# Kernel optimization log

Measured on AMD Instinct MI355X. Metric: run time of the kernel, lower is better.

## Reference

```python
import jax, jax.numpy as jnp
import numpy as np

N_PTS = 50000
EMBED = 192
HEADS = 12
HEAD_DIM = EMBED // HEADS          # 16
HPP = HEADS // 3                   # heads per strip plane = 4
QUANT = 0.25
QGL = 8                            # quant_grid_length = window/quant
TBL = 2 * QGL - 1                  # 15
BOX = 16.0
WS_XY = np.array([2.0, 2.0, 1.0], np.float32)
WS_XZ = np.array([2.0, 1.0, 2.0], np.float32)
WS_YZ = np.array([1.0, 2.0, 2.0], np.float32)


def _build_idx(xyz, ws):
    # padded per-window gather indices: equivalent of get_indices_params
    n = xyz.shape[0]
    sh = xyz - xyz.min(0)
    w = np.floor(sh / ws).astype(np.int64)
    key = (w[:, 0] * 100000 + w[:, 1]) * 100000 + w[:, 2]
    uniq, inv, counts = np.unique(key, return_inverse=True, return_counts=True)
    order = np.argsort(inv, kind='stable')
    starts = np.cumsum(counts) - counts
    pos = np.arange(n) - starts[inv[order]]
    idx = np.full((len(uniq), int(counts.max())), n, dtype=np.int32)  # pad = n
    idx[inv[order], pos] = order.astype(np.int32)
    return idx


def setup_inputs() -> dict:
    rng = np.random.default_rng(0)
    xyz = rng.uniform(0.0, BOX, (N_PTS, 3)).astype(np.float32)
    feats = rng.standard_normal((N_PTS, EMBED)).astype(np.float32)
    tbl = lambda: jnp.asarray((rng.standard_normal((TBL, 3, HPP, HEAD_DIM)) * 0.02).astype(np.float32))
    return {
        'feats': jnp.asarray(feats),
        'xyz': jnp.asarray(xyz),
        'idx_xy': jnp.asarray(_build_idx(xyz, WS_XY)),
        'idx_xz': jnp.asarray(_build_idx(xyz, WS_XZ)),
        'idx_yz': jnp.asarray(_build_idx(xyz, WS_YZ)),
        'W_qkv': jnp.asarray((rng.standard_normal((EMBED, 3 * EMBED)) * 0.02).astype(np.float32)),
        'b_qkv': jnp.zeros((3 * EMBED,), jnp.float32),
        'q_table': tbl(),
        'k_table': tbl(),
        'v_table': tbl(),
        'W_proj': jnp.asarray((rng.standard_normal((EMBED, EMBED)) * 0.02).astype(np.float32)),
        'b_proj': jnp.zeros((EMBED,), jnp.float32),
    }


def _plane_attention(q, k, v, xyz, idx, ws, qt, kt, vt):
    # q,k,v: [N,h,hd]; idx: [W,M] padded window membership (pad index == N)
    n, h, hd = q.shape
    Wn, M = idx.shape
    # quantized in-window coordinates (get_relative_position_index)
    qc = jnp.floor(((xyz - xyz.min(0)) % ws) / QUANT).astype(jnp.int32)
    pad = lambda a: jnp.concatenate([a, jnp.zeros((1,) + a.shape[1:], a.dtype)], axis=0)
    Q, K, V, QC = pad(q)[idx], pad(k)[idx], pad(v)[idx], pad(qc)[idx]
    mask = idx < n                                  # [W,M] valid slots
    rel = QC[:, :, None, :] - QC[:, None, :, :] + (QGL - 1)   # [W,M,M,3]
    logits = jnp.einsum('wmhd,wnhd->wmnh', Q, K)
    # per-slot dot products with every table row, gathered per pair
    qb = jnp.einsum('wmhd,lthd->wmtlh', Q, qt)      # [W,M,3,TBL,h]
    kb = jnp.einsum('wnhd,lthd->wntlh', K, kt)
    for t in range(3):
        r = rel[..., t]                             # [W,M,M]
        logits = logits + jnp.take_along_axis(qb[:, :, t], r[..., None], axis=2)
        rk = jnp.swapaxes(r, 1, 2)[..., None]       # index by key slot
        logits = logits + jnp.swapaxes(jnp.take_along_axis(kb[:, :, t], rk, axis=2), 1, 2)
    logits = jnp.where(mask[:, None, :, None], logits, -1e9)
    attn = jax.nn.softmax(logits, axis=2)           # [W,M,M,h]
    out = jnp.einsum('wmnh,wnhd->wmhd', attn, V)
    # relative-position value table: out_i += sum_n attn_in * v_table[rel_in]
    row = jnp.arange(Wn * M, dtype=jnp.int32).reshape(Wn, M)
    for t in range(3):
        ids = row[:, :, None] * TBL + rel[..., t]
        cb = jax.ops.segment_sum(attn.reshape(-1, h), ids.reshape(-1),
                                 num_segments=Wn * M * TBL)
        out = out + jnp.einsum('wmlh,lhd->wmhd', cb.reshape(Wn, M, TBL, h), vt[:, t])
    out = out * mask[..., None, None]
    acc = jnp.zeros((n + 1, h, hd), out.dtype).at[idx.reshape(-1)].add(out.reshape(-1, h, hd))
    return acc[:n]


def reference(feats, xyz, idx_xy, idx_xz, idx_yz, W_qkv, b_qkv,
              q_table, k_table, v_table, W_proj, b_proj):
    n = feats.shape[0]
    scale = HEAD_DIM ** -0.5
    qkv = (feats @ W_qkv + b_qkv).reshape(n, 3, HEADS, HEAD_DIM)
    q, k, v = qkv[:, 0] * scale, qkv[:, 1], qkv[:, 2]
    planes = [(idx_xy, jnp.asarray(WS_XY)), (idx_xz, jnp.asarray(WS_XZ)), (idx_yz, jnp.asarray(WS_YZ))]
    outs = []
    for p, (idx, ws) in enumerate(planes):
        sl = slice(p * HPP, (p + 1) * HPP)
        outs.append(_plane_attention(q[:, sl], k[:, sl], v[:, sl], xyz, idx, ws,
                                     q_table, k_table, v_table))
    x = jnp.concatenate(outs, axis=1).reshape(n, EMBED)
    return x @ W_proj + b_proj
```

## Files before the change

### kernel.cpp

```cpp
#include <hip/hip_runtime.h>
#include <math.h>

typedef __attribute__((ext_vector_type(8))) short bf16x8;
typedef __attribute__((ext_vector_type(4))) float f32x4;

union U16 { uint4 u; bf16x8 b; ushort s[8]; };

__device__ __forceinline__ ushort f2bf_rne(float f) {
  unsigned u = __float_as_uint(f);
  unsigned r = u + 0x7fffu + ((u >> 16) & 1u);
  return (ushort)(r >> 16);
}
__device__ __forceinline__ float bf2f(ushort h) {
  return __uint_as_float((unsigned)h << 16);
}

__global__ void min_init_kernel(unsigned* minb) {
  if (threadIdx.x < 3) minb[threadIdx.x] = 0x7f800000u;
}

__global__ void min_reduce_kernel(const float* __restrict__ xyz, unsigned* minb, int n) {
  float m0 = 1e30f, m1 = 1e30f, m2 = 1e30f;
  for (int i = blockIdx.x * blockDim.x + threadIdx.x; i < n; i += gridDim.x * blockDim.x) {
    m0 = fminf(m0, xyz[3 * i + 0]);
    m1 = fminf(m1, xyz[3 * i + 1]);
    m2 = fminf(m2, xyz[3 * i + 2]);
  }
#pragma unroll
  for (int off = 32; off > 0; off >>= 1) {
    m0 = fminf(m0, __shfl_down(m0, off, 64));
    m1 = fminf(m1, __shfl_down(m1, off, 64));
    m2 = fminf(m2, __shfl_down(m2, off, 64));
  }
  if ((threadIdx.x & 63) == 0) {
    atomicMin(&minb[0], __float_as_uint(m0));
    atomicMin(&minb[1], __float_as_uint(m1));
    atomicMin(&minb[2], __float_as_uint(m2));
  }
}

__global__ void prep_w_kernel(const float* __restrict__ W, short* __restrict__ Wh,
                              short* __restrict__ Wl, int K, int Ncols) {
  int idx = blockIdx.x * 256 + threadIdx.x;
  if (idx >= K * Ncols) return;
  int n = idx / K, k = idx - n * K;
  float v = W[(size_t)k * Ncols + n];
  ushort h = f2bf_rne(v);
  Wh[idx] = (short)h;
  Wl[idx] = (short)f2bf_rne(v - bf2f(h));
}

__global__ __launch_bounds__(256, 2) void mfma_gemm_kernel(
    const float* __restrict__ A, const short* __restrict__ Bh_g, const short* __restrict__ Bl_g,
    const float* __restrict__ bias, float* __restrict__ C, ushort* __restrict__ Cb,
    int Mrows, int Ncols, int K, int mode)
{
  __shared__ short Ah[128][40];
  __shared__ short Al[128][40];
  __shared__ short Bsh[128][40];
  __shared__ short Bsl[128][40];
  const int tid = threadIdx.x;
  const int lane = tid & 63;
  const int w = tid >> 6;
  const int wm = w >> 1, wn = w & 1;
  const int rowBase = blockIdx.y * 128;
  const int colBase = blockIdx.x * 128;

  f32x4 acc[4][4];
#pragma unroll
  for (int i = 0; i < 4; ++i)
#pragma unroll
    for (int j = 0; j < 4; ++j)
      acc[i][j] = (f32x4){0.f, 0.f, 0.f, 0.f};

  const int ma = tid >> 3;
  const int ka = (tid & 7) * 4;
  const int fr = lane & 15;
  const int kq = (lane >> 4) * 8;

  for (int k0 = 0; k0 < K; k0 += 32) {
    __syncthreads();
#pragma unroll
    for (int i = 0; i < 4; ++i) {
      int m = ma + 32 * i;
      int gr = rowBase + m;
      float4 v = make_float4(0.f, 0.f, 0.f, 0.f);
      if (gr < Mrows) v = *(const float4*)&A[(size_t)gr * K + k0 + ka];
      ushort h0 = f2bf_rne(v.x), h1 = f2bf_rne(v.y), h2 = f2bf_rne(v.z), h3 = f2bf_rne(v.w);
      ushort l0 = f2bf_rne(v.x - bf2f(h0));
      ushort l1 = f2bf_rne(v.y - bf2f(h1));
      ushort l2 = f2bf_rne(v.z - bf2f(h2));
      ushort l3 = f2bf_rne(v.w - bf2f(h3));
      uint2 hw, lw;
      hw.x = (unsigned)h0 | ((unsigned)h1 << 16);
      hw.y = (unsigned)h2 | ((unsigned)h3 << 16);
      lw.x = (unsigned)l0 | ((unsigned)l1 << 16);
      lw.y = (unsigned)l2 | ((unsigned)l3 << 16);
      *(uint2*)&Ah[m][ka] = hw;
      *(uint2*)&Al[m][ka] = lw;
    }
#pragma unroll
    for (int i = 0; i < 2; ++i) {
      int s = tid + 256 * i;
      int n = s >> 2;
      int k8 = (s & 3) * 8;
      int gn = colBase + n;
      if (gn >= Ncols) gn = Ncols - 1;
      *(uint4*)&Bsh[n][k8] = *(const uint4*)&Bh_g[(size_t)gn * K + k0 + k8];
      *(uint4*)&Bsl[n][k8] = *(const uint4*)&Bl_g[(size_t)gn * K + k0 + k8];
    }
    __syncthreads();
    bf16x8 afh[4], afl[4], bfh[4], bfl[4];
#pragma unroll
    for (int t = 0; t < 4; ++t) {
      int r = wm * 64 + t * 16 + fr;
      afh[t] = *(const bf16x8*)&Ah[r][kq];
      afl[t] = *(const bf16x8*)&Al[r][kq];
      int c = wn * 64 + t * 16 + fr;
      bfh[t] = *(const bf16x8*)&Bsh[c][kq];
      bfl[t] = *(const bf16x8*)&Bsl[c][kq];
    }
#pragma unroll
    for (int mt = 0; mt < 4; ++mt)
#pragma unroll
      for (int nt = 0; nt < 4; ++nt) {
        acc[mt][nt] = __builtin_amdgcn_mfma_f32_16x16x32_bf16(afh[mt], bfh[nt], acc[mt][nt], 0, 0, 0);
        acc[mt][nt] = __builtin_amdgcn_mfma_f32_16x16x32_bf16(afh[mt], bfl[nt], acc[mt][nt], 0, 0, 0);
        acc[mt][nt] = __builtin_amdgcn_mfma_f32_16x16x32_bf16(afl[mt], bfh[nt], acc[mt][nt], 0, 0, 0);
      }
  }
  const int cr = (lane >> 4) * 4;
  const int ccol = lane & 15;
#pragma unroll
  for (int mt = 0; mt < 4; ++mt) {
#pragma unroll
    for (int nt = 0; nt < 4; ++nt) {
      int col = colBase + wn * 64 + nt * 16 + ccol;
      if (col >= Ncols) continue;
      float bv = bias[col];
      float sc = (mode == 1 && col < 192) ? 0.25f : 1.0f;
#pragma unroll
      for (int r = 0; r < 4; ++r) {
        int row = rowBase + wm * 64 + mt * 16 + cr + r;
        if (row >= Mrows) continue;
        float val = (acc[mt][nt][r] + bv) * sc;
        if (mode == 1) Cb[(size_t)row * Ncols + col] = f2bf_rne(val);
        else C[(size_t)row * Ncols + col] = val;
      }
    }
  }
}

__global__ __launch_bounds__(256) void augment_mfma_kernel(
    const ushort* __restrict__ qkv_bf, const float* __restrict__ xyz,
    const unsigned* __restrict__ minb,
    const float* __restrict__ qt, const float* __restrict__ kt,
    ushort* __restrict__ QBg, ushort* __restrict__ KBg, ushort* __restrict__ qcg, int N)
{
  __shared__ ushort sQ[4][64 * 48 + 16];
  __shared__ ushort sKb[4][64 * 48 + 16];
  const int tid = threadIdx.x;
  const int lane = tid & 63;
  const int h = tid >> 6;
  const int p = blockIdx.y;
  const int n0 = blockIdx.x * 64;
  const int fc = lane & 15;
  const int qd = lane >> 4;

  bf16x8 tqh[3], tql[3], tkh[3], tkl[3];
#pragma unroll
  for (int ct = 0; ct < 3; ++ct) {
    U16 qh_, ql_, kh_, kl_;
    qh_.u = make_uint4(0u, 0u, 0u, 0u); ql_.u = qh_.u; kh_.u = qh_.u; kl_.u = qh_.u;
    int col = ct * 16 + fc;
    if (col < 45 && qd < 2) {
      int l = col / 3, t3 = col - l * 3;
      const float* qp = qt + (((l * 3 + t3) * 4 + h) * 16) + qd * 8;
      const float* kp = kt + (((l * 3 + t3) * 4 + h) * 16) + qd * 8;
#pragma unroll
      for (int j = 0; j < 8; ++j) {
        float qv = qp[j], kv = kp[j];
        ushort qhh = f2bf_rne(qv);
        qh_.s[j] = qhh; ql_.s[j] = f2bf_rne(qv - bf2f(qhh));
        ushort khh = f2bf_rne(kv);
        kh_.s[j] = khh; kl_.s[j] = f2bf_rne(kv - bf2f(khh));
      }
    }
    tqh[ct] = qh_.b; tql[ct] = ql_.b; tkh[ct] = kh_.b; tkl[ct] = kl_.b;
  }

#pragma unroll
  for (int mt = 0; mt < 4; ++mt) {
    int n = n0 + mt * 16 + fc;
    if (n >= N) n = N - 1;
    U16 qa, ka;
    qa.u = make_uint4(0u, 0u, 0u, 0u); ka.u = qa.u;
    if (qd < 2) {
      const ushort* base = qkv_bf + (size_t)n * 576 + p * 64 + h * 16 + qd * 8;
      qa.u = *(const uint4*)base;
      ka.u = *(const uint4*)(base + 192);
    }
#pragma unroll
    for (int ct = 0; ct < 3; ++ct) {
      f32x4 aq = (f32x4){0.f, 0.f, 0.f, 0.f}, ak = aq;
      aq = __builtin_amdgcn_mfma_f32_16x16x32_bf16(qa.b, tqh[ct], aq, 0, 0, 0);
      aq = __builtin_amdgcn_mfma_f32_16x16x32_bf16(qa.b, tql[ct], aq, 0, 0, 0);
      ak = __builtin_amdgcn_mfma_f32_16x16x32_bf16(ka.b, tkh[ct], ak, 0, 0, 0);
      ak = __builtin_amdgcn_mfma_f32_16x16x32_bf16(ka.b, tkl[ct], ak, 0, 0, 0);
#pragma unroll
      for (int i = 0; i < 4; ++i) {
        int r = mt * 16 + qd * 4 + i;
        sQ[h][r * 48 + ct * 16 + fc]  = f2bf_rne(aq[i]);
        sKb[h][r * 48 + ct * 16 + fc] = f2bf_rne(ak[i]);
      }
    }
  }
  __syncthreads();

  const int r = tid >> 2;
  const int hh = tid & 3;
  const int n = n0 + r;
  if (n >= N) return;
  const float ws0 = (p == 2) ? 1.f : 2.f;
  const float ws1 = (p == 1) ? 1.f : 2.f;
  const float ws2 = (p == 0) ? 1.f : 2.f;
  int qc[3];
  qc[0] = (int)floorf(fmodf(xyz[3 * n + 0] - __uint_as_float(minb[0]), ws0) * 4.0f);
  qc[1] = (int)floorf(fmodf(xyz[3 * n + 1] - __uint_as_float(minb[1]), ws1) * 4.0f);
  qc[2] = (int)floorf(fmodf(xyz[3 * n + 2] - __uint_as_float(minb[2]), ws2) * 4.0f);
  const size_t pN = (size_t)p * N;
  if (hh == 0) qcg[pN + n] = (ushort)(qc[0] | (qc[1] << 3) | (qc[2] << 6));

  U16 oq[3], ok[3];
#pragma unroll
  for (int t3 = 0; t3 < 3; ++t3) {
#pragma unroll
    for (int cc = 0; cc < 8; ++cc) {
      int lq = qc[t3] - cc + 7;
      int lk = cc - qc[t3] + 7;
      oq[t3].s[cc] = sQ[hh][r * 48 + lq * 3 + t3];
      ok[t3].s[cc] = sKb[hh][r * 48 + lk * 3 + t3];
    }
  }
  ushort* qo = QBg + ((pN + n) * 4 + hh) * 24;
  ushort* ko = KBg + ((pN + n) * 4 + hh) * 24;
#pragma unroll
  for (int t3 = 0; t3 < 3; ++t3) {
    *(uint4*)(qo + t3 * 8) = oq[t3].u;
    *(uint4*)(ko + t3 * 8) = ok[t3].u;
  }
}

__global__ __launch_bounds__(256, 2) void attn_mfma_kernel(
    const ushort* __restrict__ qkv_bf,
    const ushort* __restrict__ QBg, const ushort* __restrict__ KBg,
    const ushort* __restrict__ qcg,
    const int* __restrict__ idx0, const int* __restrict__ idx1, const int* __restrict__ idx2,
    int M0, int M1, int M2, int N,
    const float* __restrict__ vt,
    float* __restrict__ xout)
{
  __shared__ ushort sK[4][32][72];
  __shared__ ushort sVt[4][48][40];
  __shared__ ushort sP[4][16][56];
  __shared__ int sRows[256];
  __shared__ int s_count;

  const int p = blockIdx.y;
  const int* idx; int M;
  if (p == 0)      { idx = idx0; M = M0; }
  else if (p == 1) { idx = idx1; M = M1; }
  else             { idx = idx2; M = M2; }
  const int w = blockIdx.x;
  const int* rowp = idx + (size_t)w * M;
  const int tid = threadIdx.x;
  if (tid == 0) s_count = 0;
  __syncthreads();
  const int Mc = M < 256 ? M : 256;
  for (int s = tid; s < Mc; s += 256) {
    int g = rowp[s];
    sRows[s] = g;
    if (g < N) atomicMax(&s_count, s + 1);
  }
  __syncthreads();
  const int count = s_count;
  if (count == 0) return;

  const int lane = tid & 63;
  const int h = tid >> 6;
  const int ln = lane & 15;
  const int qd = lane >> 4;
  const size_t pN = (size_t)p * N;

  for (int qb0 = 0; qb0 < count; qb0 += 64) {
    bf16x8 qfrag[4][2];
#pragma unroll
    for (int t = 0; t < 4; ++t) {
#pragma unroll
      for (int ks = 0; ks < 2; ++ks) {
        U16 f; f.u = make_uint4(0u, 0u, 0u, 0u);
        int m = qb0 + t * 16 + ln;
        if (m < count) {
          int g = sRows[m];
          int chunk = ks * 32 + qd * 8;
          if (chunk < 16) {
            f.u = *(const uint4*)(qkv_bf + (size_t)g * 576 + p * 64 + h * 16 + chunk);
          } else if (chunk < 40) {
            f.u = *(const uint4*)(QBg + ((pN + g) * 4 + h) * 24 + (chunk - 16));
          } else {
            int t3 = (chunk - 40) >> 3;
            int qc = (qcg[pN + g] >> (3 * t3)) & 7;
            unsigned one = 0x3F80u << ((qc & 1) * 16);
            int dw = qc >> 1;
            f.u.x = dw == 0 ? one : 0u; f.u.y = dw == 1 ? one : 0u;
            f.u.z = dw == 2 ? one : 0u; f.u.w = dw == 3 ? one : 0u;
          }
        }
        qfrag[t][ks] = f.b;
      }
    }
    f32x4 O[4][3];
#pragma unroll
    for (int t = 0; t < 4; ++t)
#pragma unroll
      for (int j = 0; j < 3; ++j) O[t][j] = (f32x4){0.f, 0.f, 0.f, 0.f};

    for (int c0 = 0; c0 < count; c0 += 32) {
      const int nc = min(32, count - c0);
      __syncthreads();
      if (tid < 128) {
        const int s = tid & 31, h2 = tid >> 5;
        const bool real = s < nc;
        int g = real ? sRows[c0 + s] : 0;
        uint4 z = make_uint4(0u, 0u, 0u, 0u);
        const ushort* kr = qkv_bf + (size_t)g * 576 + 192 + p * 64 + h2 * 16;
        *(uint4*)&sK[h2][s][0] = real ? *(const uint4*)kr : z;
        *(uint4*)&sK[h2][s][8] = real ? *(const uint4*)(kr + 8) : z;
        const ushort* kb = KBg + ((pN + g) * 4 + h2) * 24;
#pragma unroll
        for (int c = 0; c < 3; ++c)
          *(uint4*)&sK[h2][s][40 + c * 8] = real ? *(const uint4*)(kb + c * 8) : z;
        unsigned qcp = real ? (unsigned)qcg[pN + g] : 0u;
#pragma unroll
        for (int t3 = 0; t3 < 3; ++t3) {
          int qc = (qcp >> (3 * t3)) & 7;
          unsigned one = real ? (0x3F80u << ((qc & 1) * 16)) : 0u;
          int dw = qc >> 1;
          uint4 o;
          o.x = dw == 0 ? one : 0u; o.y = dw == 1 ? one : 0u;
          o.z = dw == 2 ? one : 0u; o.w = dw == 3 ? one : 0u;
          *(uint4*)&sK[h2][s][16 + t3 * 8] = o;
        }
      } else {
        const int t2 = tid - 128;
        const int s = t2 & 31, h2 = t2 >> 5;
        const bool real = s < nc;
        int g = real ? sRows[c0 + s] : 0;
        U16 v0, v1;
        const ushort* vr = qkv_bf + (size_t)g * 576 + 384 + p * 64 + h2 * 16;
        v0.u = real ? *(const uint4*)vr : make_uint4(0u, 0u, 0u, 0u);
        v1.u = real ? *(const uint4*)(vr + 8) : make_uint4(0u, 0u, 0u, 0u);
#pragma unroll
        for (int j = 0; j < 8; ++j) {
          sVt[h2][j][s] = v0.s[j];
          sVt[h2][8 + j][s] = v1.s[j];
        }
        unsigned qcp = real ? (unsigned)qcg[pN + g] : 0u;
#pragma unroll
        for (int t3 = 0; t3 < 3; ++t3) {
          int qc = (qcp >> (3 * t3)) & 7;
#pragma unroll
          for (int cc = 0; cc < 8; ++cc)
            sVt[h2][16 + t3 * 8 + cc][s] = (real && cc == qc) ? (ushort)0x3F80 : (ushort)0;
        }
        sVt[h2][40][s] = real ? (ushort)0x3F80 : (ushort)0;
#pragma unroll
        for (int c = 41; c < 48; ++c) sVt[h2][c][s] = 0;
      }
      __syncthreads();
      bf16x8 kfrag[2][2], vfrag[3];
#pragma unroll
      for (int j = 0; j < 2; ++j)
#pragma unroll
        for (int ks = 0; ks < 2; ++ks)
          kfrag[j][ks] = *(const bf16x8*)&sK[h][j * 16 + ln][ks * 32 + qd * 8];
#pragma unroll
      for (int j = 0; j < 3; ++j)
        vfrag[j] = *(const bf16x8*)&sVt[h][j * 16 + ln][qd * 8];
#pragma unroll
      for (int t = 0; t < 4; ++t) {
        if (qb0 + t * 16 >= count) break;
        f32x4 a0 = (f32x4){0.f, 0.f, 0.f, 0.f}, a1 = a0;
        a0 = __builtin_amdgcn_mfma_f32_16x16x32_bf16(qfrag[t][0], kfrag[0][0], a0, 0, 0, 0);
        a0 = __builtin_amdgcn_mfma_f32_16x16x32_bf16(qfrag[t][1], kfrag[0][1], a0, 0, 0, 0);
        a1 = __builtin_amdgcn_mfma_f32_16x16x32_bf16(qfrag[t][0], kfrag[1][0], a1, 0, 0, 0);
        a1 = __builtin_amdgcn_mfma_f32_16x16x32_bf16(qfrag[t][1], kfrag[1][1], a1, 0, 0, 0);
#pragma unroll
        for (int i = 0; i < 4; ++i) {
          sP[h][qd * 4 + i][ln]      = f2bf_rne(__expf(a0[i]));
          sP[h][qd * 4 + i][16 + ln] = f2bf_rne(__expf(a1[i]));
        }
        asm volatile("s_waitcnt lgkmcnt(0)" ::: "memory");
        bf16x8 pf = *(const bf16x8*)&sP[h][ln][qd * 8];
#pragma unroll
        for (int j = 0; j < 3; ++j)
          O[t][j] = __builtin_amdgcn_mfma_f32_16x16x32_bf16(pf, vfrag[j], O[t][j], 0, 0, 0);
        asm volatile("s_waitcnt lgkmcnt(0)" ::: "memory");
      }
    }
    float* sE = (float*)&sK[h][0][0];
#pragma unroll
    for (int t = 0; t < 4; ++t) {
      if (qb0 + t * 16 >= count) break;
#pragma unroll
      for (int j = 0; j < 3; ++j)
#pragma unroll
        for (int i = 0; i < 4; ++i)
          sE[(qd * 4 + i) * 52 + j * 16 + ln] = O[t][j][i];
      asm volatile("s_waitcnt lgkmcnt(0)" ::: "memory");
      int m = qb0 + t * 16 + ln;
      if (m < count) {
        int g = sRows[m];
        int d0 = qd * 4;
        float denom = sE[ln * 52 + 40];
        float4 acc = *(float4*)&sE[ln * 52 + d0];
        unsigned qcp = qcg[pN + g];
#pragma unroll
        for (int t3 = 0; t3 < 3; ++t3) {
          int qc = (qcp >> (3 * t3)) & 7;
#pragma unroll
          for (int cc = 0; cc < 8; ++cc) {
            float mass = sE[ln * 52 + 16 + t3 * 8 + cc];
            const float* vp = vt + (((size_t)(qc - cc + 7) * 3 + t3) * 4 + h) * 16 + d0;
            float4 v4 = *(const float4*)vp;
            acc.x += mass * v4.x; acc.y += mass * v4.y;
            acc.z += mass * v4.z; acc.w += mass * v4.w;
          }
        }
        float inv = 1.f / denom;
        float4 o = make_float4(acc.x * inv, acc.y * inv, acc.z * inv, acc.w * inv);
        *(float4*)&xout[(size_t)g * 192 + (p * 4 + h) * 16 + d0] = o;
      }
      asm volatile("s_waitcnt lgkmcnt(0)" ::: "memory");
    }
  }
}

extern "C" void kernel_launch(void* const* d_in, const int* in_sizes, int n_in,
                              void* d_out, int out_size, void* d_ws, size_t ws_size,
                              hipStream_t stream)
{
  const float* feats  = (const float*)d_in[0];
  const float* xyz    = (const float*)d_in[1];
  const int*   idx_xy = (const int*)d_in[2];
  const int*   idx_xz = (const int*)d_in[3];
  const int*   idx_yz = (const int*)d_in[4];
  const float* W_qkv  = (const float*)d_in[5];
  const float* b_qkv  = (const float*)d_in[6];
  const float* qt     = (const float*)d_in[7];
  const float* kt     = (const float*)d_in[8];
  const float* vt     = (const float*)d_in[9];
  const float* W_proj = (const float*)d_in[10];
  const float* b_proj = (const float*)d_in[11];

  const int N  = in_sizes[0] / 192;
  const int Wn = 1024;
  const int M0 = in_sizes[2] / Wn;
  const int M1 = in_sizes[3] / Wn;
  const int M2 = in_sizes[4] / Wn;

  size_t off = 0;
  char* base = (char*)d_ws;
  auto alloc = [&](size_t bytes) -> void* {
    void* ptr = base + off;
    off += (bytes + 15) & ~(size_t)15;
    return ptr;
  };
  ushort*   qkv_bf = (ushort*)alloc((size_t)N * 576 * 2);
  float*    xbuf   = (float*)alloc((size_t)N * 192 * 4);
  unsigned* minb   = (unsigned*)alloc(16);
  ushort*   QBg    = (ushort*)alloc((size_t)3 * N * 96 * 2);
  ushort*   KBg    = (ushort*)alloc((size_t)3 * N * 96 * 2);
  ushort*   qcg    = (ushort*)alloc((size_t)3 * N * 2);
  short*    wtq_h  = (short*)alloc((size_t)576 * 192 * 2);
  short*    wtq_l  = (short*)alloc((size_t)576 * 192 * 2);
  short*    wtp_h  = (short*)alloc((size_t)192 * 192 * 2);
  short*    wtp_l  = (short*)alloc((size_t)192 * 192 * 2);

  min_init_kernel<<<1, 64, 0, stream>>>(minb);
  min_reduce_kernel<<<64, 256, 0, stream>>>(xyz, minb, N);

  prep_w_kernel<<<(576 * 192 + 255) / 256, 256, 0, stream>>>(W_qkv, wtq_h, wtq_l, 192, 576);
  prep_w_kernel<<<(192 * 192 + 255) / 256, 256, 0, stream>>>(W_proj, wtp_h, wtp_l, 192, 192);

  {
    dim3 grid((576 + 127) / 128, (N + 127) / 128);
    mfma_gemm_kernel<<<grid, 256, 0, stream>>>(feats, wtq_h, wtq_l, b_qkv,
                                               (float*)nullptr, qkv_bf, N, 576, 192, 1);
  }
  {
    dim3 grid((N + 63) / 64, 3);
    augment_mfma_kernel<<<grid, 256, 0, stream>>>(qkv_bf, xyz, minb, qt, kt, QBg, KBg, qcg, N);
  }
  {
    dim3 grid(Wn, 3);
    attn_mfma_kernel<<<grid, 256, 0, stream>>>(qkv_bf, QBg, KBg, qcg,
                                               idx_xy, idx_xz, idx_yz,
                                               M0, M1, M2, N, vt, xbuf);
  }
  {
    dim3 grid((192 + 127) / 128, (N + 127) / 128);
    mfma_gemm_kernel<<<grid, 256, 0, stream>>>(xbuf, wtp_h, wtp_l, b_proj,
                                               (float*)d_out, (ushort*)nullptr, N, 192, 192, 0);
  }
}
```

Baseline: 438.9 us.

## Make attention wavefront-local: load K fragments directly, drop block barriers

Each wavefront now loads its own head's K fragments straight from global memory into registers, removing the shared K tile. It also stages only its own head's transposed V slice in shared memory. With per-head data private to a wave, the two block-wide barriers per key chunk are gone, and exp/P writes for all query tiles are batched before the PV MFMAs. The launch-bounds occupancy hint is dropped and the P buffer is enlarged to hold all four tiles. In exchange, K loads are issued redundantly per lane and scattered global reads may expose more latency.

```diff
diff --git a/kernel.cpp b/kernel.cpp
--- a/kernel.cpp
+++ b/kernel.cpp
@@ -251,7 +251,7 @@
   }
 }
 
-__global__ __launch_bounds__(256, 2) void attn_mfma_kernel(
+__global__ __launch_bounds__(256) void attn_mfma_kernel(
     const ushort* __restrict__ qkv_bf,
     const ushort* __restrict__ QBg, const ushort* __restrict__ KBg,
     const ushort* __restrict__ qcg,
@@ -260,9 +260,8 @@
     const float* __restrict__ vt,
     float* __restrict__ xout)
 {
-  __shared__ ushort sK[4][32][72];
   __shared__ ushort sVt[4][48][40];
-  __shared__ ushort sP[4][16][56];
+  __shared__ ushort sP[4][64][40];
   __shared__ int sRows[256];
   __shared__ int s_count;
 
@@ -290,6 +289,8 @@
   const int h = tid >> 6;
   const int ln = lane & 15;
   const int qd = lane >> 4;
+  const int vs = lane & 31;
+  const int vhalf = lane >> 5;
   const size_t pN = (size_t)p * N;
 
   for (int qb0 = 0; qb0 < count; qb0 += 64) {
@@ -319,6 +320,8 @@
         qfrag[t][ks] = f.b;
       }
     }
+    const int ntile = (count - qb0 < 64) ? ((count - qb0 + 15) >> 4) : 4;
+
     f32x4 O[4][3];
 #pragma unroll
     for (int t = 0; t < 4; ++t)
@@ -326,70 +329,63 @@
       for (int j = 0; j < 3; ++j) O[t][j] = (f32x4){0.f, 0.f, 0.f, 0.f};
 
     for (int c0 = 0; c0 < count; c0 += 32) {
-      const int nc = min(32, count - c0);
-      __syncthreads();
-      if (tid < 128) {
-        const int s = tid & 31, h2 = tid >> 5;
-        const bool real = s < nc;
-        int g = real ? sRows[c0 + s] : 0;
-        uint4 z = make_uint4(0u, 0u, 0u, 0u);
-        const ushort* kr = qkv_bf + (size_t)g * 576 + 192 + p * 64 + h2 * 16;
-        *(uint4*)&sK[h2][s][0] = real ? *(const uint4*)kr : z;
-        *(uint4*)&sK[h2][s][8] = real ? *(const uint4*)(kr + 8) : z;
-        const ushort* kb = KBg + ((pN + g) * 4 + h2) * 24;
-#pragma unroll
-        for (int c = 0; c < 3; ++c)
-          *(uint4*)&sK[h2][s][40 + c * 8] = real ? *(const uint4*)(kb + c * 8) : z;
+      {
+        int nn = c0 + vs;
+        bool real = nn < count;
+        int g = real ? sRows[nn] : 0;
+        U16 v0;
+        v0.u = real ? *(const uint4*)(qkv_bf + (size_t)g * 576 + 384 + p * 64 + h * 16 + vhalf * 8)
+                    : make_uint4(0u, 0u, 0u, 0u);
         unsigned qcp = real ? (unsigned)qcg[pN + g] : 0u;
 #pragma unroll
-        for (int t3 = 0; t3 < 3; ++t3) {
-          int qc = (qcp >> (3 * t3)) & 7;
-          unsigned one = real ? (0x3F80u << ((qc & 1) * 16)) : 0u;
-          int dw = qc >> 1;
-          uint4 o;
-          o.x = dw == 0 ? one : 0u; o.y = dw == 1 ? one : 0u;
-          o.z = dw == 2 ? one : 0u; o.w = dw == 3 ? one : 0u;
-          *(uint4*)&sK[h2][s][16 + t3 * 8] = o;
+        for (int j = 0; j < 8; ++j)
+          sVt[h][vhalf * 8 + j][vs] = v0.s[j];
+        if (vhalf == 0) {
+          int qc = qcp & 7;
+#pragma unroll
+          for (int cc = 0; cc < 8; ++cc)
+            sVt[h][16 + cc][vs] = (real && cc == qc) ? (ushort)0x3F80 : (ushort)0;
+          sVt[h][40][vs] = real ? (ushort)0x3F80 : (ushort)0;
+#pragma unroll
+          for (int c = 41; c < 48; ++c) sVt[h][c][vs] = 0;
+        } else {
+          int qc1 = (qcp >> 3) & 7, qc2 = (qcp >> 6) & 7;
+#pragma unroll
+          for (int cc = 0; cc < 8; ++cc) {
+            sVt[h][24 + cc][vs] = (real && cc == qc1) ? (ushort)0x3F80 : (ushort)0;
+            sVt[h][32 + cc][vs] = (real && cc == qc2) ? (ushort)0x3F80 : (ushort)0;
+          }
         }
-      } else {
-        const int t2 = tid - 128;
-        const int s = t2 & 31, h2 = t2 >> 5;
-        const bool real = s < nc;
-        int g = real ? sRows[c0 + s] : 0;
-        U16 v0, v1;
-        const ushort* vr = qkv_bf + (size_t)g * 576 + 384 + p * 64 + h2 * 16;
-        v0.u = real ? *(const uint4*)vr : make_uint4(0u, 0u, 0u, 0u);
-        v1.u = real ? *(const uint4*)(vr + 8) : make_uint4(0u, 0u, 0u, 0u);
-#pragma unroll
-        for (int j = 0; j < 8; ++j) {
-          sVt[h2][j][s] = v0.s[j];
-          sVt[h2][8 + j][s] = v1.s[j];
+      }
+      bf16x8 kfrag[2][2];
+#pragma unroll
+      for (int j = 0; j < 2; ++j) {
+        int nn = c0 + j * 16 + ln;
+        bool real = nn < count;
+        int g = real ? sRows[nn] : 0;
+#pragma unroll
+        for (int ks = 0; ks < 2; ++ks) {
+          U16 f; f.u = make_uint4(0u, 0u, 0u, 0u);
+          if (real) {
+            int chunk = ks * 32 + qd * 8;
+            if (chunk < 16) {
+              f.u = *(const uint4*)(qkv_bf + (size_t)g * 576 + 192 + p * 64 + h * 16 + chunk);
+            } else if (chunk < 40) {
+              int t3 = (chunk - 16) >> 3;
+              int qc = (qcg[pN + g] >> (3 * t3)) & 7;
+              unsigned one = 0x3F80u << ((qc & 1) * 16);
+              int dw = qc >> 1;
+              f.u.x = dw == 0 ? one : 0u; f.u.y = dw == 1 ? one : 0u;
+              f.u.z = dw == 2 ? one : 0u; f.u.w = dw == 3 ? one : 0u;
+            } else {
+              f.u = *(const uint4*)(KBg + ((pN + g) * 4 + h) * 24 + (chunk - 40));
+            }
+          }
+          kfrag[j][ks] = f.b;
         }
-        unsigned qcp = real ? (unsigned)qcg[pN + g] : 0u;
-#pragma unroll
-        for (int t3 = 0; t3 < 3; ++t3) {
-          int qc = (qcp >> (3 * t3)) & 7;
-#pragma unroll
-          for (int cc = 0; cc < 8; ++cc)
-            sVt[h2][16 + t3 * 8 + cc][s] = (real && cc == qc) ? (ushort)0x3F80 : (ushort)0;
-        }
-        sVt[h2][40][s] = real ? (ushort)0x3F80 : (ushort)0;
-#pragma unroll
-        for (int c = 41; c < 48; ++c) sVt[h2][c][s] = 0;
-      }
-      __syncthreads();
-      bf16x8 kfrag[2][2], vfrag[3];
-#pragma unroll
-      for (int j = 0; j < 2; ++j)
-#pragma unroll
-        for (int ks = 0; ks < 2; ++ks)
-          kfrag[j][ks] = *(const bf16x8*)&sK[h][j * 16 + ln][ks * 32 + qd * 8];
-#pragma unroll
-      for (int j = 0; j < 3; ++j)
-        vfrag[j] = *(const bf16x8*)&sVt[h][j * 16 + ln][qd * 8];
-#pragma unroll
-      for (int t = 0; t < 4; ++t) {
-        if (qb0 + t * 16 >= count) break;
+      }
+      asm volatile("s_waitcnt lgkmcnt(0)" ::: "memory");
+      for (int t = 0; t < ntile; ++t) {
         f32x4 a0 = (f32x4){0.f, 0.f, 0.f, 0.f}, a1 = a0;
         a0 = __builtin_amdgcn_mfma_f32_16x16x32_bf16(qfrag[t][0], kfrag[0][0], a0, 0, 0, 0);
         a0 = __builtin_amdgcn_mfma_f32_16x16x32_bf16(qfrag[t][1], kfrag[0][1], a0, 0, 0, 0);
@@ -397,21 +393,25 @@
         a1 = __builtin_amdgcn_mfma_f32_16x16x32_bf16(qfrag[t][1], kfrag[1][1], a1, 0, 0, 0);
 #pragma unroll
         for (int i = 0; i < 4; ++i) {
-          sP[h][qd * 4 + i][ln]      = f2bf_rne(__expf(a0[i]));
-          sP[h][qd * 4 + i][16 + ln] = f2bf_rne(__expf(a1[i]));
+          sP[h][t * 16 + qd * 4 + i][ln]      = f2bf_rne(__expf(a0[i]));
+          sP[h][t * 16 + qd * 4 + i][16 + ln] = f2bf_rne(__expf(a1[i]));
         }
-        asm volatile("s_waitcnt lgkmcnt(0)" ::: "memory");
-        bf16x8 pf = *(const bf16x8*)&sP[h][ln][qd * 8];
+      }
+      asm volatile("s_waitcnt lgkmcnt(0)" ::: "memory");
+      bf16x8 vfrag[3];
+#pragma unroll
+      for (int j = 0; j < 3; ++j)
+        vfrag[j] = *(const bf16x8*)&sVt[h][j * 16 + ln][qd * 8];
+      for (int t = 0; t < ntile; ++t) {
+        bf16x8 pf = *(const bf16x8*)&sP[h][t * 16 + ln][qd * 8];
 #pragma unroll
         for (int j = 0; j < 3; ++j)
           O[t][j] = __builtin_amdgcn_mfma_f32_16x16x32_bf16(pf, vfrag[j], O[t][j], 0, 0, 0);
-        asm volatile("s_waitcnt lgkmcnt(0)" ::: "memory");
-      }
-    }
-    float* sE = (float*)&sK[h][0][0];
-#pragma unroll
-    for (int t = 0; t < 4; ++t) {
-      if (qb0 + t * 16 >= count) break;
+      }
+      asm volatile("s_waitcnt lgkmcnt(0)" ::: "memory");
+    }
+    float* sE = (float*)&sP[h][0][0];
+    for (int t = 0; t < ntile; ++t) {
 #pragma unroll
       for (int j = 0; j < 3; ++j)
 #pragma unroll
```

After: 1.122 ms. +155.7%, slower.

## Compute value-table epilogue with MFMA on bf16 hi/lo split tables

Applied to the files above, without the earlier changes.

The per-query scalar epilogue loop over relative-position value tables is replaced by scattering the mass terms into a relative-index mask matrix in LDS. That matrix is multiplied on MFMA against the value table, which is pre-split into bf16 high and low parts and held in registers. The change also packs the P stores into 32-bit words, permutes the V-transpose row mapping, caches per-query quantised coordinates in LDS, and drops the occupancy hint from launch bounds. It aims to remove the serial global table reads and FMAs in the epilogue, at the cost of more registers and a bf16 rounding of the mass values.

```diff
diff --git a/kernel.cpp b/kernel.cpp
--- a/kernel.cpp
+++ b/kernel.cpp
@@ -251,7 +251,7 @@
   }
 }
 
-__global__ __launch_bounds__(256, 2) void attn_mfma_kernel(
+__global__ __launch_bounds__(256) void attn_mfma_kernel(
     const ushort* __restrict__ qkv_bf,
     const ushort* __restrict__ QBg, const ushort* __restrict__ KBg,
     const ushort* __restrict__ qcg,
@@ -260,9 +260,11 @@
     const float* __restrict__ vt,
     float* __restrict__ xout)
 {
-  __shared__ ushort sK[4][32][72];
-  __shared__ ushort sVt[4][48][40];
-  __shared__ ushort sP[4][16][56];
+  __shared__ __align__(16) ushort sK[4][32][72];
+  __shared__ __align__(16) ushort sVt[4][48][40];
+  __shared__ __align__(16) ushort sP[4][16][40];
+  __shared__ __align__(16) ushort sQcH[4][64];
+  __shared__ float sDen[4][16];
   __shared__ int sRows[256];
   __shared__ int s_count;
 
@@ -291,6 +293,27 @@
   const int ln = lane & 15;
   const int qd = lane >> 4;
   const size_t pN = (size_t)p * N;
+
+  bf16x8 vth[2], vtl[2];
+#pragma unroll
+  for (int ks = 0; ks < 2; ++ks) {
+    U16 hi, lo;
+    hi.u = make_uint4(0u, 0u, 0u, 0u); lo.u = hi.u;
+#pragma unroll
+    for (int j = 0; j < 8; ++j) {
+      int k = ks * 32 + qd * 8 + j;
+      if (k < 48) {
+        int t3 = k >> 4, l = k & 15;
+        if (l < 15) {
+          float v = vt[(((size_t)l * 3 + t3) * 4 + h) * 16 + ln];
+          ushort hh = f2bf_rne(v);
+          hi.s[j] = hh;
+          lo.s[j] = f2bf_rne(v - bf2f(hh));
+        }
+      }
+    }
+    vth[ks] = hi.b; vtl[ks] = lo.b;
+  }
 
   for (int qb0 = 0; qb0 < count; qb0 += 64) {
     bf16x8 qfrag[4][2];
@@ -319,6 +342,16 @@
         qfrag[t][ks] = f.b;
       }
     }
+    if (qd == 0) {
+#pragma unroll
+      for (int t = 0; t < 4; ++t) {
+        int m = qb0 + t * 16 + ln;
+        ushort qcp = 0;
+        if (m < count) qcp = qcg[pN + sRows[m]];
+        sQcH[h][t * 16 + ln] = qcp;
+      }
+    }
+
     f32x4 O[4][3];
 #pragma unroll
     for (int t = 0; t < 4; ++t)
@@ -354,8 +387,9 @@
       } else {
         const int t2 = tid - 128;
         const int s = t2 & 31, h2 = t2 >> 5;
-        const bool real = s < nc;
-        int g = real ? sRows[c0 + s] : 0;
+        const int pr = ((s & 1) << 4) | (s >> 1);
+        const bool real = pr < nc;
+        int g = real ? sRows[c0 + pr] : 0;
         U16 v0, v1;
         const ushort* vr = qkv_bf + (size_t)g * 576 + 384 + p * 64 + h2 * 16;
         v0.u = real ? *(const uint4*)vr : make_uint4(0u, 0u, 0u, 0u);
@@ -397,8 +431,9 @@
         a1 = __builtin_amdgcn_mfma_f32_16x16x32_bf16(qfrag[t][1], kfrag[1][1], a1, 0, 0, 0);
 #pragma unroll
         for (int i = 0; i < 4; ++i) {
-          sP[h][qd * 4 + i][ln]      = f2bf_rne(__expf(a0[i]));
-          sP[h][qd * 4 + i][16 + ln] = f2bf_rne(__expf(a1[i]));
+          unsigned pw = (unsigned)f2bf_rne(__expf(a0[i])) |
+                        ((unsigned)f2bf_rne(__expf(a1[i])) << 16);
+          ((unsigned*)&sP[h][qd * 4 + i][0])[ln] = pw;
         }
         asm volatile("s_waitcnt lgkmcnt(0)" ::: "memory");
         bf16x8 pf = *(const bf16x8*)&sP[h][ln][qd * 8];
@@ -408,38 +443,48 @@
         asm volatile("s_waitcnt lgkmcnt(0)" ::: "memory");
       }
     }
-    float* sE = (float*)&sK[h][0][0];
+    ushort* maskA = &sK[h][0][0];
 #pragma unroll
     for (int t = 0; t < 4; ++t) {
       if (qb0 + t * 16 >= count) break;
 #pragma unroll
-      for (int j = 0; j < 3; ++j)
-#pragma unroll
-        for (int i = 0; i < 4; ++i)
-          sE[(qd * 4 + i) * 52 + j * 16 + ln] = O[t][j][i];
+      for (int z = 0; z < 3; ++z)
+        *(uint2*)&maskA[(lane * 3 + z) * 4] = make_uint2(0u, 0u);
       asm volatile("s_waitcnt lgkmcnt(0)" ::: "memory");
-      int m = qb0 + t * 16 + ln;
-      if (m < count) {
-        int g = sRows[m];
-        int d0 = qd * 4;
-        float denom = sE[ln * 52 + 40];
-        float4 acc = *(float4*)&sE[ln * 52 + d0];
-        unsigned qcp = qcg[pN + g];
-#pragma unroll
-        for (int t3 = 0; t3 < 3; ++t3) {
-          int qc = (qcp >> (3 * t3)) & 7;
-#pragma unroll
-          for (int cc = 0; cc < 8; ++cc) {
-            float mass = sE[ln * 52 + 16 + t3 * 8 + cc];
-            const float* vp = vt + (((size_t)(qc - cc + 7) * 3 + t3) * 4 + h) * 16 + d0;
-            float4 v4 = *(const float4*)vp;
-            acc.x += mass * v4.x; acc.y += mass * v4.y;
-            acc.z += mass * v4.z; acc.w += mass * v4.w;
-          }
-        }
-        float inv = 1.f / denom;
-        float4 o = make_float4(acc.x * inv, acc.y * inv, acc.z * inv, acc.w * inv);
-        *(float4*)&xout[(size_t)g * 192 + (p * 4 + h) * 16 + d0] = o;
+#pragma unroll
+      for (int i = 0; i < 4; ++i) {
+        int row = qd * 4 + i;
+        ushort qcp = sQcH[h][t * 16 + row];
+        {
+          int t3 = ln >> 3, cc = ln & 7;
+          int l = ((qcp >> (3 * t3)) & 7) - cc + 7;
+          maskA[row * 48 + t3 * 16 + l] = f2bf_rne(O[t][1][i]);
+        }
+        if (ln < 8) {
+          int l = ((qcp >> 6) & 7) - ln + 7;
+          maskA[row * 48 + 32 + l] = f2bf_rne(O[t][2][i]);
+        } else if (ln == 8) {
+          sDen[h][row] = O[t][2][i];
+        }
+      }
+      asm volatile("s_waitcnt lgkmcnt(0)" ::: "memory");
+      U16 a1r, a2r;
+      a1r.u = *(const uint4*)&maskA[ln * 48 + qd * 8];
+      a2r.u = make_uint4(0u, 0u, 0u, 0u);
+      if (qd < 2) a2r.u = *(const uint4*)&maskA[ln * 48 + 32 + qd * 8];
+      f32x4 ob = O[t][0];
+      ob = __builtin_amdgcn_mfma_f32_16x16x32_bf16(a1r.b, vth[0], ob, 0, 0, 0);
+      ob = __builtin_amdgcn_mfma_f32_16x16x32_bf16(a1r.b, vtl[0], ob, 0, 0, 0);
+      ob = __builtin_amdgcn_mfma_f32_16x16x32_bf16(a2r.b, vth[1], ob, 0, 0, 0);
+      ob = __builtin_amdgcn_mfma_f32_16x16x32_bf16(a2r.b, vtl[1], ob, 0, 0, 0);
+#pragma unroll
+      for (int i = 0; i < 4; ++i) {
+        int row = qd * 4 + i;
+        int m = qb0 + t * 16 + row;
+        if (m < count) {
+          float inv = 1.0f / sDen[h][row];
+          xout[(size_t)sRows[m] * 192 + (p * 4 + h) * 16 + ln] = ob[i] * inv;
+        }
       }
       asm volatile("s_waitcnt lgkmcnt(0)" ::: "memory");
     }
```

After: 416.3 us. -5.2%, faster.
